# Kernel optimization log

Hardware: AMD Instinct MI355X
Metric: run time of the kernel (lower is better)

Reference implementation:

```python
import jax, jax.numpy as jnp
from jax import lax
import numpy as np

# pywt db4 decomposition filters (8 taps)
DEC_LO = np.array([-0.010597401785069032, 0.0328830116668852, 0.030841381835560764,
                   -0.18703481171909309, -0.027983769416859854, 0.6308807679298589,
                   0.7148465705529157, 0.2303778133088965], dtype=np.float32)
DEC_HI = np.array([-0.2303778133088965, 0.7148465705529157, -0.6308807679298589,
                   -0.027983769416859854, 0.18703481171909309, 0.030841381835560764,
                   -0.0328830116668852, -0.010597401785069032], dtype=np.float32)

LEVELS = 5
POOL = 128       # adaptive pool size inside each WaveletLevelNet
LEVEL_HID = 128  # per-level net output dim
OUT_DIM = 512
BATCH, SIGLEN = 2048, 16384


def dwt_step(a, filt):
    """One DWT level. a: [B, n]; filt: [2, L] (dec_lo, dec_hi).
    pywt-style: symmetric pad, full convolution, downsample at odd indices.
    Output length = floor((n + L - 1)/2)."""
    L = filt.shape[-1]
    xp = jnp.pad(a, ((0, 0), (L - 2, L - 1)), mode='symmetric')[:, None, :]  # [B,1,n+2L-3]
    k = filt[:, ::-1][:, None, :]  # flip -> true convolution; [2,1,L]
    out = lax.conv_general_dilated(xp, k, (2,), 'VALID',
                                   dimension_numbers=('NCH', 'OIH', 'NCH'))  # [B,2,m]
    return out[:, 0, :], out[:, 1, :]  # cA, cD


def wavedec(x, levels):
    filt = jnp.stack([jnp.asarray(DEC_LO), jnp.asarray(DEC_HI)])
    a = x
    details = []
    for _ in range(levels):  # small fixed loop over levels
        a, d = dwt_step(a, filt)
        details.append(d)
    return [a] + details[::-1]  # [cA_L, cD_L, cD_{L-1}, ..., cD_1]


def adaptive_avg_pool(x, P):
    """torch AdaptiveAvgPool1d over last dim via cumsum segment means."""
    n = x.shape[-1]
    idx = np.arange(P)
    starts = (idx * n) // P
    ends = ((idx + 1) * n + P - 1) // P
    cs = jnp.cumsum(x, axis=-1)
    cs = jnp.concatenate([jnp.zeros_like(cs[..., :1]), cs], axis=-1)
    return (cs[..., ends] - cs[..., starts]) / jnp.asarray(ends - starts, x.dtype)


def setup_inputs() -> dict:
    key = jax.random.key(0)
    k0, k1, k2 = jax.random.split(key, 3)
    x = jax.random.normal(k0, (BATCH, SIGLEN), dtype=jnp.float32)
    level_w = jax.random.normal(k1, (LEVELS, LEVEL_HID, POOL), dtype=jnp.float32) * 0.05
    level_b = jnp.zeros((LEVELS, LEVEL_HID), dtype=jnp.float32)
    fusion_w = jax.random.normal(k2, (OUT_DIM, LEVELS * LEVEL_HID), dtype=jnp.float32) * 0.05
    fusion_b = jnp.zeros((OUT_DIM,), dtype=jnp.float32)
    return {"x": x, "level_w": level_w, "level_b": level_b,
            "fusion_w": fusion_w, "fusion_b": fusion_b}


def reference(x, level_w, level_b, fusion_w, fusion_b):
    coeffs = wavedec(x, LEVELS)  # 6 arrays; forward uses the first 5
    pooled = jnp.stack([adaptive_avg_pool(coeffs[i], POOL) for i in range(LEVELS)])  # [5,B,P]
    feats = jax.nn.relu(jnp.einsum('lbp,lop->lbo', pooled, level_w) + level_b[:, None, :])
    comb = jnp.transpose(feats, (1, 0, 2)).reshape(x.shape[0], LEVELS * LEVEL_HID)  # [B,640]
    return jax.nn.relu(comb @ fusion_w.T + fusion_b)  # Dropout is identity in eval
```

## Files before the change

kernel.cpp:

```cpp
#include <hip/hip_runtime.h>


#define BATCH   2048
#define SIGLEN  16384
#define N1      8195
#define N2      4101
#define N3      2054
#define N4      1030
#define N5      518
#define POOLP   128
#define COMB    640
#define OUTD    512
#define WLEN    400

typedef __fp16 h2 __attribute__((ext_vector_type(2)));

__device__ constexpr float LO[8] = {
     0.2303778133088965f,   0.7148465705529157f,   0.6308807679298589f,
    -0.027983769416859854f, -0.18703481171909309f,  0.030841381835560764f,
     0.0328830116668852f,  -0.010597401785069032f };
__device__ constexpr float HI[8] = {
    -0.010597401785069032f, -0.0328830116668852f,   0.030841381835560764f,
     0.18703481171909309f,  -0.027983769416859854f, -0.6308807679298589f,
     0.7148465705529157f,  -0.2303778133088965f };

__global__ __launch_bounds__(128) void build_w(h2* __restrict__ wt,
                                               int2* __restrict__ meta)
{
    __shared__ float g0[512], g1[512];
    const int c = blockIdx.x;
    const int slot = c >> 7, p = c & 127;
    const int tid = threadIdx.x;

    const int bandN[5] = {N5, N5, N4, N3, N2};
    const int M = bandN[slot];
    const int s = (p * M) >> 7;
    const int e = ((p + 1) * M + 127) >> 7;

    for (int i = tid; i < 512; i += 128) { g0[i] = 0.f; g1[i] = 0.f; }
    __syncthreads();
    const float inv = 1.f / (float)(e - s);
    for (int i = tid; i < e - s; i += 128) g0[i] = inv;
    __syncthreads();

    float* cur = g0;
    float* nxt = g1;
    int ws = s, we = e;

    const int nsteps = (slot <= 1) ? 5 : (6 - slot);
    const int nins[5] = {N4, N3, N2, N1, SIGLEN};
    const int start = 5 - nsteps;

    for (int st = 0; st < nsteps; ++st) {
        const int Nin = nins[start + st];
        const bool useHI = (st == 0 && slot >= 1);
        const int nws = (2 * ws - 6 < 0) ? 0 : (2 * ws - 6);
        const int nwe = (2 * we < Nin) ? (2 * we) : Nin;
        for (int i = tid; i < nwe - nws; i += 128) nxt[i] = 0.f;
        __syncthreads();
        for (int t = 0; t < 8; ++t) {
            const float f = useHI ? HI[t] : LO[t];
            for (int j = ws + tid; j < we; j += 128) {
                int idx = 2 * j - 6 + t;
                idx = (idx < 0) ? (-1 - idx) : idx;
                idx = (idx >= Nin) ? (2 * Nin - 1 - idx) : idx;
                nxt[idx - nws] += f * cur[j - ws];
            }
            __syncthreads();
        }
        float* tmp = cur; cur = nxt; nxt = tmp;
        ws = nws; we = nwe;
    }

    const int sx0 = ws & ~7;
    const int len = we - sx0;
    const int nk = (len + 7) >> 3;
    if (tid == 0) meta[c] = make_int2(sx0, nk);
    __fp16* wrow = reinterpret_cast<__fp16*>(wt + (size_t)c * (WLEN / 2));
    for (int i = tid; i < WLEN; i += 128) {
        const int idx = sx0 + i;
        const float v = (idx >= ws && idx < we) ? cur[idx - ws] : 0.f;
        wrow[i] = (__fp16)v;
    }
}

__global__ __launch_bounds__(512) void banded_kernel(const float* __restrict__ x,
                                                     const h2* __restrict__ wt,
                                                     const int2* __restrict__ meta,
                                                     float* __restrict__ pooled) {
    __shared__ __align__(16) unsigned int xs_u[SIGLEN / 2 + 4];
    const int tid = threadIdx.x;
    const int row = blockIdx.x;
    const float* __restrict__ xr = x + (size_t)row * SIGLEN;

    for (int i = tid; i < SIGLEN / 4; i += 512) {
        const float4 v = *reinterpret_cast<const float4*>(xr + 4 * i);
        const h2 p0 = __builtin_amdgcn_cvt_pkrtz(v.x, v.y);
        const h2 p1 = __builtin_amdgcn_cvt_pkrtz(v.z, v.w);
        uint2 pk;
        pk.x = __builtin_bit_cast(unsigned int, p0);
        pk.y = __builtin_bit_cast(unsigned int, p1);
        *reinterpret_cast<uint2*>(xs_u + 2 * i) = pk;
    }
    if (tid < 4) xs_u[SIGLEN / 2 + tid] = 0u;
    __syncthreads();

    const float* __restrict__ xs_f = reinterpret_cast<const float*>(xs_u);
    const int sub = tid & 7;
    const int cb  = tid >> 3;

#pragma unroll
    for (int pass = 0; pass < 10; ++pass) {
        const int c = pass * 64 + cb;
        const int2 m = meta[c];
        const int sxh = m.x >> 1;
        const int nk = m.y;
        const h2* __restrict__ wrow = wt + (size_t)c * (WLEN / 2);
        float acc = 0.f;
        for (int g = sub; g < nk; g += 8) {
            const float4 xv = *reinterpret_cast<const float4*>(xs_f + sxh + 4 * g);
            const float4 wv = *reinterpret_cast<const float4*>(wrow + 4 * g);
            acc = __builtin_amdgcn_fdot2(__builtin_bit_cast(h2, xv.x), __builtin_bit_cast(h2, wv.x), acc, false);
            acc = __builtin_amdgcn_fdot2(__builtin_bit_cast(h2, xv.y), __builtin_bit_cast(h2, wv.y), acc, false);
            acc = __builtin_amdgcn_fdot2(__builtin_bit_cast(h2, xv.z), __builtin_bit_cast(h2, wv.z), acc, false);
            acc = __builtin_amdgcn_fdot2(__builtin_bit_cast(h2, xv.w), __builtin_bit_cast(h2, wv.w), acc, false);
        }
        acc += __shfl_xor(acc, 1);
        acc += __shfl_xor(acc, 2);
        acc += __shfl_xor(acc, 4);
        if (sub == 0) pooled[(size_t)row * COMB + c] = acc;
    }
}


#define SWZ(i) ((i) ^ ((((i) >> 5) & 7) << 2))
#define NTHR 512

__device__ __forceinline__ int symfold(int idx, int n) {
    idx = (idx < 0) ? (-1 - idx) : idx;
    idx = (idx >= n) ? (2 * n - 1 - idx) : idx;
    return idx;
}
constexpr int cmin(int a, int b) { return a < b ? a : b; }
constexpr int cmax(int a, int b) { return a > b ? a : b; }

template<int SS, int SE, int BSRC, int NSRC, int S, int E, int BDST>
__device__ __forceinline__ void dwt_chunk(const float* __restrict__ src,
                                          float* __restrict__ dstA,
                                          float* __restrict__ dstD, int tid) {
    for (int j0 = (S & ~3) + tid * 4; j0 < E; j0 += NTHR * 4) {
        const int rb = 2 * j0 - 8;
        if ((rb >= SS) && (2 * j0 + 7 <= SE - 1) && (j0 + 4 <= E)) {
            const int lrb = rb - BSRC;
            const float4 v0 = *reinterpret_cast<const float4*>(src + SWZ(lrb));
            const float4 v1 = *reinterpret_cast<const float4*>(src + SWZ(lrb + 4));
            const float4 v2 = *reinterpret_cast<const float4*>(src + SWZ(lrb + 8));
            const float4 v3 = *reinterpret_cast<const float4*>(src + SWZ(lrb + 12));
            float w[16];
            w[0]=v0.x;  w[1]=v0.y;  w[2]=v0.z;  w[3]=v0.w;
            w[4]=v1.x;  w[5]=v1.y;  w[6]=v1.z;  w[7]=v1.w;
            w[8]=v2.x;  w[9]=v2.y;  w[10]=v2.z; w[11]=v2.w;
            w[12]=v3.x; w[13]=v3.y; w[14]=v3.z; w[15]=v3.w;
            float a[4], d[4];
#pragma unroll
            for (int k = 0; k < 4; ++k) {
                float aa = 0.f, dd = 0.f;
#pragma unroll
                for (int t = 0; t < 8; ++t) {
                    const float v = w[2 + 2 * k + t];
                    aa = fmaf(v, LO[t], aa);
                    dd = fmaf(v, HI[t], dd);
                }
                a[k] = aa; d[k] = dd;
            }
            const int ds = j0 - BDST;
            *reinterpret_cast<float4*>(dstA + SWZ(ds)) = make_float4(a[0], a[1], a[2], a[3]);
            *reinterpret_cast<float4*>(dstD + SWZ(ds)) = make_float4(d[0], d[1], d[2], d[3]);
        } else {
            for (int k = 0; k < 4; ++k) {
                const int j = j0 + k;
                if (j < S || j >= E) continue;
                float aa = 0.f, dd = 0.f;
#pragma unroll
                for (int t = 0; t < 8; ++t) {
                    const int idx = symfold(2 * j - 6 + t, NSRC);
                    const float v = src[SWZ(idx - BSRC)];
                    aa = fmaf(v, LO[t], aa);
                    dd = fmaf(v, HI[t], dd);
                }
                dstA[SWZ(j - BDST)] = aa;
                dstD[SWZ(j - BDST)] = dd;
            }
        }
    }
}

template<int S, int E, int BDST>
__device__ __forceinline__ void dwt_l1(const float* __restrict__ xr,
                                       float* __restrict__ dstA, int tid) {
    for (int j0 = (S & ~3) + tid * 4; j0 < E; j0 += NTHR * 4) {
        const int rb = 2 * j0 - 8;
        if ((rb >= 0) && (2 * j0 + 7 <= SIGLEN - 1) && (j0 + 4 <= E)) {
            const float4* s4 = reinterpret_cast<const float4*>(xr + rb);
            const float4 v0 = s4[0], v1 = s4[1], v2 = s4[2], v3 = s4[3];
            float w[16];
            w[0]=v0.x;  w[1]=v0.y;  w[2]=v0.z;  w[3]=v0.w;
            w[4]=v1.x;  w[5]=v1.y;  w[6]=v1.z;  w[7]=v1.w;
            w[8]=v2.x;  w[9]=v2.y;  w[10]=v2.z; w[11]=v2.w;
            w[12]=v3.x; w[13]=v3.y; w[14]=v3.z; w[15]=v3.w;
            float a[4];
#pragma unroll
            for (int k = 0; k < 4; ++k) {
                float aa = 0.f;
#pragma unroll
                for (int t = 0; t < 8; ++t) aa = fmaf(w[2 + 2 * k + t], LO[t], aa);
                a[k] = aa;
            }
            *reinterpret_cast<float4*>(dstA + SWZ(j0 - BDST)) = make_float4(a[0], a[1], a[2], a[3]);
        } else {
            for (int k = 0; k < 4; ++k) {
                const int j = j0 + k;
                if (j < S || j >= E) continue;
                float aa = 0.f;
#pragma unroll
                for (int t = 0; t < 8; ++t) {
                    const int idx = symfold(2 * j - 6 + t, SIGLEN);
                    aa = fmaf(xr[idx], LO[t], aa);
                }
                dstA[SWZ(j - BDST)] = aa;
            }
        }
    }
}

template<int N, int BASE, int P0>
__device__ __forceinline__ void pool64(const float* __restrict__ buf,
                                       float* __restrict__ dst, int tid) {
    const int p = P0 + (tid >> 3), sub = tid & 7;
    const int s = (p * N) >> 7;
    const int e = ((p + 1) * N + 127) >> 7;
    float acc = 0.f;
    for (int t = s + sub; t < e; t += 8) acc += buf[SWZ(t - BASE)];
    acc += __shfl_xor(acc, 1);
    acc += __shfl_xor(acc, 2);
    acc += __shfl_xor(acc, 4);
    if (sub == 0) dst[p] = acc / (float)(e - s);
}

template<int B>
__device__ __forceinline__ void dwt_body(const float* __restrict__ xr,
                                         float* __restrict__ pr,
                                         float* __restrict__ A, float* __restrict__ Bb,
                                         float* __restrict__ D1, float* __restrict__ D2,
                                         int tid) {
    constexpr int p0 = B * 64;
    constexpr int sP5 = (p0 * N5) >> 7, eP5 = ((p0 + 64) * N5 + 127) >> 7;
    constexpr int sP4 = (p0 * N4) >> 7, eP4 = ((p0 + 64) * N4 + 127) >> 7;
    constexpr int sP3 = (p0 * N3) >> 7, eP3 = ((p0 + 64) * N3 + 127) >> 7;
    constexpr int sP2 = (p0 * N2) >> 7, eP2 = ((p0 + 64) * N2 + 127) >> 7;
    constexpr int s5 = sP5, e5 = cmin(eP5, N5);
    constexpr int s4 = cmax(cmin(sP4, 2 * s5 - 6), 0);
    constexpr int e4 = cmin(cmax(eP4, 2 * e5), N4);
    constexpr int s3 = cmax(cmin(sP3, 2 * s4 - 6), 0);
    constexpr int e3 = cmin(cmax(eP3, 2 * e4), N3);
    constexpr int s2 = cmax(cmin(sP2, 2 * s3 - 6), 0);
    constexpr int e2 = cmin(cmax(eP2, 2 * e3), N2);
    constexpr int s1 = cmax(2 * s2 - 6, 0);
    constexpr int e1 = cmin(2 * e2, N1);
    constexpr int b1 = (s1 & ~3) - 8, b2 = (s2 & ~3) - 8, b3 = (s3 & ~3) - 8;
    constexpr int b4 = (s4 & ~3) - 8, b5 = (s5 & ~3) - 8;

    dwt_l1<s1, e1, b1>(xr, A, tid);
    __syncthreads();
    dwt_chunk<s1, e1, b1, N1, s2, e2, b2>(A, Bb, D1, tid);
    __syncthreads();
    dwt_chunk<s2, e2, b2, N2, s3, e3, b3>(Bb, A, D2, tid);
    pool64<N2, b2, p0>(D1, pr + 4 * POOLP, tid);
    __syncthreads();
    dwt_chunk<s3, e3, b3, N3, s4, e4, b4>(A, Bb, D1, tid);
    pool64<N3, b3, p0>(D2, pr + 3 * POOLP, tid);
    __syncthreads();
    dwt_chunk<s4, e4, b4, N4, s5, e5, b5>(Bb, A, D2, tid);
    pool64<N4, b4, p0>(D1, pr + 2 * POOLP, tid);
    __syncthreads();
    pool64<N5, b5, p0>(A,  pr + 0 * POOLP, tid);
    pool64<N5, b5, p0>(D2, pr + 1 * POOLP, tid);
}

__global__ __launch_bounds__(NTHR, 4) void dwt_pool_kernel(const float* __restrict__ x,
                                                           float* __restrict__ pooled) {
    __shared__ __align__(16) float A[4192];
    __shared__ __align__(16) float Bb[2144];
    __shared__ __align__(16) float D1[2144];
    __shared__ __align__(16) float D2[1088];
    const int tid = threadIdx.x;
    const int row = blockIdx.x >> 1;
    const float* __restrict__ xr = x + (size_t)row * SIGLEN;
    float* __restrict__ pr = pooled + (size_t)row * COMB;
    if (blockIdx.x & 1) dwt_body<1>(xr, pr, A, Bb, D1, D2, tid);
    else                dwt_body<0>(xr, pr, A, Bb, D1, D2, tid);
}


#define LW_PAIRS (5 * 128 * 128 / 2)
#define FW_PAIRS (512 * 640 / 2)

__global__ __launch_bounds__(256) void pack_w(const float* __restrict__ lw,
                                              const float* __restrict__ fw,
                                              h2* __restrict__ lwh,
                                              h2* __restrict__ fwh) {
    const int i = blockIdx.x * 256 + threadIdx.x;
    if (i < LW_PAIRS) {
        const float2 v = reinterpret_cast<const float2*>(lw)[i];
        lwh[i] = __builtin_amdgcn_cvt_pkrtz(v.x, v.y);
    } else if (i < LW_PAIRS + FW_PAIRS) {
        const float2 v = reinterpret_cast<const float2*>(fw)[i - LW_PAIRS];
        fwh[i - LW_PAIRS] = __builtin_amdgcn_cvt_pkrtz(v.x, v.y);
    }
}

__global__ __launch_bounds__(1024, 4) void mlp_kernel(const float* __restrict__ pooled,
                                                      const h2* __restrict__ lwh,
                                                      const float* __restrict__ lb,
                                                      const h2* __restrict__ fwh,
                                                      const float* __restrict__ fb,
                                                      float* __restrict__ out) {
    __shared__ h2 sph[8][COMB / 2];
    __shared__ h2 sch[8][COMB / 2];
    const int tid = threadIdx.x;
    const int r0 = blockIdx.x * 8;

    const float2* __restrict__ srcp = reinterpret_cast<const float2*>(pooled + (size_t)r0 * COMB);
    for (int i = tid; i < 8 * (COMB / 2); i += 1024) {
        const float2 v = srcp[i];
        (&sph[0][0])[i] = __builtin_amdgcn_cvt_pkrtz(v.x, v.y);
    }
    __syncthreads();

    for (int idx = tid; idx < COMB * 2; idx += 1024) {
        const int c = idx >> 1, rh = (idx & 1) * 4;
        const h2* __restrict__ w = lwh + (size_t)c * 64;
        const int lb2 = (c >> 7) * 64;
        const float bias = lb[c];
        float acc[4] = {bias, bias, bias, bias};
        for (int t2 = 0; t2 < 64; t2 += 4) {
            const float4 wraw = *reinterpret_cast<const float4*>(w + t2);
            const h2 w0 = __builtin_bit_cast(h2, wraw.x);
            const h2 w1 = __builtin_bit_cast(h2, wraw.y);
            const h2 w2 = __builtin_bit_cast(h2, wraw.z);
            const h2 w3 = __builtin_bit_cast(h2, wraw.w);
#pragma unroll
            for (int r = 0; r < 4; ++r) {
                const float4 praw = *reinterpret_cast<const float4*>(&sph[rh + r][lb2 + t2]);
                acc[r] = __builtin_amdgcn_fdot2(__builtin_bit_cast(h2, praw.x), w0, acc[r], false);
                acc[r] = __builtin_amdgcn_fdot2(__builtin_bit_cast(h2, praw.y), w1, acc[r], false);
                acc[r] = __builtin_amdgcn_fdot2(__builtin_bit_cast(h2, praw.z), w2, acc[r], false);
                acc[r] = __builtin_amdgcn_fdot2(__builtin_bit_cast(h2, praw.w), w3, acc[r], false);
            }
        }
        __fp16* __restrict__ schf = reinterpret_cast<__fp16*>(&sch[0][0]);
#pragma unroll
        for (int r = 0; r < 4; ++r) schf[(rh + r) * COMB + c] = (__fp16)fmaxf(acc[r], 0.f);
    }
    __syncthreads();

    {
        const int c = tid >> 1, rh = (tid & 1) * 4;
        const h2* __restrict__ w = fwh + (size_t)c * (COMB / 2);
        const float bias = fb[c];
        float acc[4] = {bias, bias, bias, bias};
        for (int t2 = 0; t2 < COMB / 2; t2 += 4) {
            const float4 wraw = *reinterpret_cast<const float4*>(w + t2);
            const h2 w0 = __builtin_bit_cast(h2, wraw.x);
            const h2 w1 = __builtin_bit_cast(h2, wraw.y);
            const h2 w2 = __builtin_bit_cast(h2, wraw.z);
            const h2 w3 = __builtin_bit_cast(h2, wraw.w);
#pragma unroll
            for (int r = 0; r < 4; ++r) {
                const float4 craw = *reinterpret_cast<const float4*>(&sch[rh + r][t2]);
                acc[r] = __builtin_amdgcn_fdot2(__builtin_bit_cast(h2, craw.x), w0, acc[r], false);
                acc[r] = __builtin_amdgcn_fdot2(__builtin_bit_cast(h2, craw.y), w1, acc[r], false);
                acc[r] = __builtin_amdgcn_fdot2(__builtin_bit_cast(h2, craw.z), w2, acc[r], false);
                acc[r] = __builtin_amdgcn_fdot2(__builtin_bit_cast(h2, craw.w), w3, acc[r], false);
            }
        }
#pragma unroll
        for (int r = 0; r < 4; ++r) {
            out[(size_t)(r0 + rh + r) * OUTD + c] = fmaxf(acc[r], 0.f);
        }
    }
}

__global__ __launch_bounds__(512) void mlp_kernel_fb(const float* __restrict__ pooled,
                                                     const float* __restrict__ lw,
                                                     const float* __restrict__ lb,
                                                     const float* __restrict__ fw,
                                                     const float* __restrict__ fb,
                                                     float* __restrict__ out) {
    __shared__ h2 sph[8][COMB / 2];
    __shared__ h2 sch[8][COMB / 2];
    const int tid = threadIdx.x;
    const int r0 = blockIdx.x * 8;
    const float2* __restrict__ srcp = reinterpret_cast<const float2*>(pooled + (size_t)r0 * COMB);
    for (int i = tid; i < 8 * (COMB / 2); i += 512) {
        const float2 v = srcp[i];
        (&sph[0][0])[i] = __builtin_amdgcn_cvt_pkrtz(v.x, v.y);
    }
    __syncthreads();
    for (int c = tid; c < COMB; c += 512) {
        const float* __restrict__ w = lw + (size_t)c * POOLP;
        const int lb2 = (c >> 7) * (POOLP / 2);
        const float bias = lb[c];
        float acc[8];
#pragma unroll
        for (int r = 0; r < 8; ++r) acc[r] = bias;
        for (int t2 = 0; t2 < POOLP / 2; t2 += 4) {
            const float4 wa = *reinterpret_cast<const float4*>(w + t2 * 2);
            const float4 wb = *reinterpret_cast<const float4*>(w + t2 * 2 + 4);
            const h2 w0 = __builtin_amdgcn_cvt_pkrtz(wa.x, wa.y);
            const h2 w1 = __builtin_amdgcn_cvt_pkrtz(wa.z, wa.w);
            const h2 w2 = __builtin_amdgcn_cvt_pkrtz(wb.x, wb.y);
            const h2 w3 = __builtin_amdgcn_cvt_pkrtz(wb.z, wb.w);
#pragma unroll
            for (int r = 0; r < 8; ++r) {
                const float4 raw = *reinterpret_cast<const float4*>(&sph[r][lb2 + t2]);
                acc[r] = __builtin_amdgcn_fdot2(__builtin_bit_cast(h2, raw.x), w0, acc[r], false);
                acc[r] = __builtin_amdgcn_fdot2(__builtin_bit_cast(h2, raw.y), w1, acc[r], false);
                acc[r] = __builtin_amdgcn_fdot2(__builtin_bit_cast(h2, raw.z), w2, acc[r], false);
                acc[r] = __builtin_amdgcn_fdot2(__builtin_bit_cast(h2, raw.w), w3, acc[r], false);
            }
        }
        __fp16* __restrict__ schf = reinterpret_cast<__fp16*>(&sch[0][0]);
#pragma unroll
        for (int r = 0; r < 8; ++r) schf[r * COMB + c] = (__fp16)fmaxf(acc[r], 0.f);
    }
    __syncthreads();
    {
        const int j = tid;
        const float* __restrict__ w = fw + (size_t)j * COMB;
        const float bias = fb[j];
        float acc[8];
#pragma unroll
        for (int r = 0; r < 8; ++r) acc[r] = bias;
        for (int t2 = 0; t2 < COMB / 2; t2 += 4) {
            const float4 wa = *reinterpret_cast<const float4*>(w + t2 * 2);
            const float4 wb = *reinterpret_cast<const float4*>(w + t2 * 2 + 4);
            const h2 w0 = __builtin_amdgcn_cvt_pkrtz(wa.x, wa.y);
            const h2 w1 = __builtin_amdgcn_cvt_pkrtz(wa.z, wa.w);
            const h2 w2 = __builtin_amdgcn_cvt_pkrtz(wb.x, wb.y);
            const h2 w3 = __builtin_amdgcn_cvt_pkrtz(wb.z, wb.w);
#pragma unroll
            for (int r = 0; r < 8; ++r) {
                const float4 raw = *reinterpret_cast<const float4*>(&sch[r][t2]);
                acc[r] = __builtin_amdgcn_fdot2(__builtin_bit_cast(h2, raw.x), w0, acc[r], false);
                acc[r] = __builtin_amdgcn_fdot2(__builtin_bit_cast(h2, raw.y), w1, acc[r], false);
                acc[r] = __builtin_amdgcn_fdot2(__builtin_bit_cast(h2, raw.z), w2, acc[r], false);
                acc[r] = __builtin_amdgcn_fdot2(__builtin_bit_cast(h2, raw.w), w3, acc[r], false);
            }
        }
#pragma unroll
        for (int r = 0; r < 8; ++r) {
            out[(size_t)(r0 + r) * OUTD + j] = fmaxf(acc[r], 0.f);
        }
    }
}

extern "C" void kernel_launch(void* const* d_in, const int* in_sizes, int n_in,
                              void* d_out, int out_size, void* d_ws, size_t ws_size,
                              hipStream_t stream) {
    const float* x  = (const float*)d_in[0];
    const float* lw = (const float*)d_in[1];
    const float* lb = (const float*)d_in[2];
    const float* fw = (const float*)d_in[3];
    const float* fb = (const float*)d_in[4];
    float* out = (float*)d_out;

    char* base = (char*)d_ws;
    const size_t POOLED_B = (size_t)BATCH * COMB * 4;
    const size_t LWH_B    = (size_t)LW_PAIRS * 4;
    const size_t FWH_B    = (size_t)FW_PAIRS * 4;
    const size_t META_B   = (size_t)COMB * 8;
    const size_t WT_B     = (size_t)COMB * WLEN * 2;

    float* pooled = (float*)base;
    h2*   lwh  = (h2*)(base + POOLED_B);
    h2*   fwh  = (h2*)(base + POOLED_B + LWH_B);
    int2* meta = (int2*)(base + POOLED_B + LWH_B + FWH_B);
    h2*   wt   = (h2*)(base + POOLED_B + LWH_B + FWH_B + META_B);

    const size_t NEED_MLP    = POOLED_B + LWH_B + FWH_B;
    const size_t NEED_BANDED = NEED_MLP + META_B + WT_B;

    if (ws_size >= NEED_BANDED) {
        build_w<<<COMB, 128, 0, stream>>>(wt, meta);
        banded_kernel<<<BATCH, 512, 0, stream>>>(x, wt, meta, pooled);
    } else {
        dwt_pool_kernel<<<BATCH * 2, NTHR, 0, stream>>>(x, pooled);
    }

    if (ws_size >= NEED_MLP) {
        pack_w<<<(LW_PAIRS + FW_PAIRS + 255) / 256, 256, 0, stream>>>(lw, fw, lwh, fwh);
        mlp_kernel<<<BATCH / 8, 1024, 0, stream>>>(pooled, lwh, lb, fwh, fb, out);
    } else {
        mlp_kernel_fb<<<BATCH / 8, 512, 0, stream>>>(pooled, lw, lb, fw, fb, out);
    }
}
```

Baseline: 102.9 us.

## Stage banded pooling weights through LDS with register prefetch and fixed-length rows

Pads every banded weight row to a fixed 512 halfs so the inner loop is fully unrolled with 16 lanes per output instead of 8, and recomputes each row's start offset instead of loading metadata. Weights for 32 outputs are staged into LDS per pass, with the next tile prefetched into registers while the current one is consumed. This removes scattered global weight reads and loop-bound divergence, but adds two block barriers per pass, extra LDS that may lower occupancy, and wasted multiply-adds on the zero padding.

```diff
diff --git a/kernel.cpp b/kernel.cpp
--- a/kernel.cpp
+++ b/kernel.cpp
@@ -11,7 +11,7 @@
 #define POOLP   128
 #define COMB    640
 #define OUTD    512
-#define WLEN    400
+#define WLEN    512
 
 typedef __fp16 h2 __attribute__((ext_vector_type(2)));
 
@@ -24,8 +24,7 @@
      0.18703481171909309f,  -0.027983769416859854f, -0.6308807679298589f,
      0.7148465705529157f,  -0.2303778133088965f };
 
-__global__ __launch_bounds__(128) void build_w(h2* __restrict__ wt,
-                                               int2* __restrict__ meta)
+__global__ __launch_bounds__(128) void build_w(h2* __restrict__ wt)
 {
     __shared__ float g0[512], g1[512];
     const int c = blockIdx.x;
@@ -73,9 +72,6 @@
     }
 
     const int sx0 = ws & ~7;
-    const int len = we - sx0;
-    const int nk = (len + 7) >> 3;
-    if (tid == 0) meta[c] = make_int2(sx0, nk);
     __fp16* wrow = reinterpret_cast<__fp16*>(wt + (size_t)c * (WLEN / 2));
     for (int i = tid; i < WLEN; i += 128) {
         const int idx = sx0 + i;
@@ -86,9 +82,10 @@
 
 __global__ __launch_bounds__(512) void banded_kernel(const float* __restrict__ x,
                                                      const h2* __restrict__ wt,
-                                                     const int2* __restrict__ meta,
                                                      float* __restrict__ pooled) {
-    __shared__ __align__(16) unsigned int xs_u[SIGLEN / 2 + 4];
+    __shared__ __align__(16) unsigned int xs_u[SIGLEN / 2 + 256];
+    __shared__ __align__(16) float wtile[32 * (WLEN / 2)];
+
     const int tid = threadIdx.x;
     const int row = blockIdx.x;
     const float* __restrict__ xr = x + (size_t)row * SIGLEN;
@@ -102,24 +99,47 @@
         pk.y = __builtin_bit_cast(unsigned int, p1);
         *reinterpret_cast<uint2*>(xs_u + 2 * i) = pk;
     }
-    if (tid < 4) xs_u[SIGLEN / 2 + tid] = 0u;
+    if (tid < 256) xs_u[SIGLEN / 2 + tid] = 0u;
+
+    {
+        const float4* src = reinterpret_cast<const float4*>(wt);
+        float4* dst = reinterpret_cast<float4*>(wtile);
+#pragma unroll
+        for (int k = 0; k < 4; ++k) dst[tid + 512 * k] = src[tid + 512 * k];
+    }
     __syncthreads();
 
     const float* __restrict__ xs_f = reinterpret_cast<const float*>(xs_u);
-    const int sub = tid & 7;
-    const int cb  = tid >> 3;
-
-#pragma unroll
-    for (int pass = 0; pass < 10; ++pass) {
-        const int c = pass * 64 + cb;
-        const int2 m = meta[c];
-        const int sxh = m.x >> 1;
-        const int nk = m.y;
-        const h2* __restrict__ wrow = wt + (size_t)c * (WLEN / 2);
+    const int sub = tid & 15;
+    const int cb  = tid >> 4;
+
+    for (int pass = 0; pass < 20; ++pass) {
+        float4 st[4];
+        const bool more = (pass < 19);
+        if (more) {
+            const float4* nsrc = reinterpret_cast<const float4*>(wt + (size_t)(pass + 1) * 8192);
+#pragma unroll
+            for (int k = 0; k < 4; ++k) st[k] = nsrc[tid + 512 * k];
+        }
+
+        const int c = pass * 32 + cb;
+        const int slot = c >> 7, p = c & 127;
+        const int M = (slot <= 1) ? N5 : (slot == 2 ? N4 : (slot == 3 ? N3 : N2));
+        const int nst = (slot <= 1) ? 5 : (6 - slot);
+        int ws = (p * M) >> 7;
+#pragma unroll
+        for (int k = 0; k < 5; ++k) {
+            if (k < nst) { int t = 2 * ws - 6; ws = (t < 0) ? 0 : t; }
+        }
+        const int sxh = (ws & ~7) >> 1;
+
         float acc = 0.f;
-        for (int g = sub; g < nk; g += 8) {
+        const float* wrow_f = wtile + cb * (WLEN / 2);
+#pragma unroll
+        for (int i = 0; i < 4; ++i) {
+            const int g = sub + 16 * i;
             const float4 xv = *reinterpret_cast<const float4*>(xs_f + sxh + 4 * g);
-            const float4 wv = *reinterpret_cast<const float4*>(wrow + 4 * g);
+            const float4 wv = *reinterpret_cast<const float4*>(wrow_f + 4 * g);
             acc = __builtin_amdgcn_fdot2(__builtin_bit_cast(h2, xv.x), __builtin_bit_cast(h2, wv.x), acc, false);
             acc = __builtin_amdgcn_fdot2(__builtin_bit_cast(h2, xv.y), __builtin_bit_cast(h2, wv.y), acc, false);
             acc = __builtin_amdgcn_fdot2(__builtin_bit_cast(h2, xv.z), __builtin_bit_cast(h2, wv.z), acc, false);
@@ -128,7 +148,16 @@
         acc += __shfl_xor(acc, 1);
         acc += __shfl_xor(acc, 2);
         acc += __shfl_xor(acc, 4);
+        acc += __shfl_xor(acc, 8);
         if (sub == 0) pooled[(size_t)row * COMB + c] = acc;
+
+        __syncthreads();
+        if (more) {
+            float4* dst = reinterpret_cast<float4*>(wtile);
+#pragma unroll
+            for (int k = 0; k < 4; ++k) dst[tid + 512 * k] = st[k];
+        }
+        __syncthreads();
     }
 }
 
@@ -479,21 +508,19 @@
     const size_t POOLED_B = (size_t)BATCH * COMB * 4;
     const size_t LWH_B    = (size_t)LW_PAIRS * 4;
     const size_t FWH_B    = (size_t)FW_PAIRS * 4;
-    const size_t META_B   = (size_t)COMB * 8;
     const size_t WT_B     = (size_t)COMB * WLEN * 2;
 
     float* pooled = (float*)base;
-    h2*   lwh  = (h2*)(base + POOLED_B);
-    h2*   fwh  = (h2*)(base + POOLED_B + LWH_B);
-    int2* meta = (int2*)(base + POOLED_B + LWH_B + FWH_B);
-    h2*   wt   = (h2*)(base + POOLED_B + LWH_B + FWH_B + META_B);
+    h2*  lwh  = (h2*)(base + POOLED_B);
+    h2*  fwh  = (h2*)(base + POOLED_B + LWH_B);
+    h2*  wt   = (h2*)(base + POOLED_B + LWH_B + FWH_B);
 
     const size_t NEED_MLP    = POOLED_B + LWH_B + FWH_B;
-    const size_t NEED_BANDED = NEED_MLP + META_B + WT_B;
+    const size_t NEED_BANDED = NEED_MLP + WT_B;
 
     if (ws_size >= NEED_BANDED) {
-        build_w<<<COMB, 128, 0, stream>>>(wt, meta);
-        banded_kernel<<<BATCH, 512, 0, stream>>>(x, wt, meta, pooled);
+        build_w<<<COMB, 128, 0, stream>>>(wt);
+        banded_kernel<<<BATCH, 512, 0, stream>>>(x, wt, pooled);
     } else {
         dwt_pool_kernel<<<BATCH * 2, NTHR, 0, stream>>>(x, pooled);
     }
```

Result: slower. 371.6 us (+261.1%).
